# Kernel optimization log

Measured on AMD Instinct MI355X. Metric: run time of the kernel, lower is better.

The kernel has to match this reference:

```python
import jax, jax.numpy as jnp
import numpy as np

B, S, D = 8, 4096, 128


def setup_inputs() -> dict:
    key = jax.random.key(0)
    kx, kw = jax.random.split(key)
    x = jax.random.normal(kx, (B, S, D), dtype=jnp.float32)
    W = jax.random.normal(kw, (D, D), dtype=jnp.float32) * 0.05  # 'random_normal' init
    b = jnp.zeros((D,), dtype=jnp.float32)  # created in build() but unused in call()
    return {"x": x, "W": W, "b": b}


def reference(x, W, b):
    # q = a = x @ W  (both projections use the same weight in the source)
    q = jnp.einsum("bsd,de->bse", x, W)
    # scores = q @ a^T -> [B, S, S]; no 1/sqrt(d) scaling in the source
    scores = jnp.einsum("bsd,btd->bst", q, q)
    attn = jax.nn.softmax(scores, axis=-1)
    # output = attn @ inputs (values are the raw inputs, not a projection)
    out = jnp.einsum("bst,btd->bsd", attn, x)
    return out
```

## Files before the change

### kernel.cpp

```cpp
#include <hip/hip_runtime.h>

typedef unsigned short u16;
typedef unsigned int u32;
typedef short s16x8 __attribute__((ext_vector_type(8)));
typedef float f32x4 __attribute__((ext_vector_type(4)));
typedef float f32x16 __attribute__((ext_vector_type(16)));

#define B_  8
#define S_  4096
#define D_  128
#define SOFF 40.0f

#define VOFF  9216
#define BUFSZ 19456
#define SBUF  (2 * BUFSZ)
#define LDSZ  (4 * SBUF)

__device__ __forceinline__ u16 f2bf(float f) {
  union { float f; unsigned u; } v; v.f = f;
  unsigned r = v.u + 0x7fffu + ((v.u >> 16) & 1u);
  return (u16)(r >> 16);
}

__device__ __forceinline__ u32 pack_bf(float a, float b) {
  union { float f; u32 u; } ua, ub;
  ua.f = a; ub.f = b;
  return ((ua.u + 0x8000u) & 0xffff0000u) | ((ub.u + 0x8000u) >> 16);
}

__device__ __forceinline__ void async_cp16(const void* g, void* l) {
  __builtin_amdgcn_global_load_lds(
      (const __attribute__((address_space(1))) void*)g,
      (__attribute__((address_space(3))) void*)l, 16, 0, 0);
}

__global__ __launch_bounds__(256) void wprep_kernel(
    const float* __restrict__ W, u16* __restrict__ wtT)
{
  __shared__ u16 wb[128][136];
  int tid = threadIdx.x;
#pragma unroll
  for (int i = 0; i < 16; ++i) {
    int idx = i * 1024 + tid * 4;
    const float* p = W + idx;
    float a = p[0], b = p[1], c = p[2], d = p[3];
    int k = idx >> 7, n = idx & 127;
    *(u32*)(&wb[k][n])     = (u32)f2bf(a) | ((u32)f2bf(b) << 16);
    *(u32*)(&wb[k][n + 2]) = (u32)f2bf(c) | ((u32)f2bf(d) << 16);
  }
  __syncthreads();
#pragma unroll
  for (int i = 0; i < 32; ++i) {
    int oi = i * 256 + tid;
    int n = oi >> 6, kp = oi & 63;
    u32 v = (u32)wb[2 * kp][n] | ((u32)wb[2 * kp + 1][n] << 16);
    ((u32*)wtT)[n * 64 + kp] = v;
  }
}

__global__ __launch_bounds__(256) void prep_kernel(
    const float* __restrict__ x, const u16* __restrict__ wtT,
    u16* __restrict__ qb, u16* __restrict__ vT)
{
  __shared__ u16 xb[32][136];
  __shared__ u16 qs[32][136];
  const int tid  = threadIdx.x;
  const int b    = blockIdx.x & 7;
  const int m0   = (blockIdx.x >> 3) * 32;
  const int lane = tid & 63, wave = tid >> 6;
  const int l32  = lane & 31, hi = lane >> 5;

  const float* xg = x + ((size_t)b * S_ + m0) * D_;
#pragma unroll
  for (int i = 0; i < 4; ++i) {
    int idx = (i * 256 + tid) * 4;
    f32x4 v = *(const f32x4*)(xg + idx);
    int row = idx >> 7, col = idx & 127;
    *(u32*)(&xb[row][col])     = (u32)f2bf(v.x) | ((u32)f2bf(v.y) << 16);
    *(u32*)(&xb[row][col + 2]) = (u32)f2bf(v.z) | ((u32)f2bf(v.w) << 16);
  }
  __syncthreads();

  u16* vTb = vT + (size_t)b * D_ * S_;
#pragma unroll
  for (int i = 0; i < 8; ++i) {
    int oi = i * 256 + tid;
    int d = oi >> 4, jj = oi & 15, t = 2 * jj;
    u32 v = (u32)xb[t][d] | ((u32)xb[t + 1][d] << 16);
    int jjs = (jj & 9) | ((jj & 2) << 1) | ((jj & 4) >> 1);
    ((u32*)(vTb + (size_t)d * S_ + m0))[jjs] = v;
  }

  s16x8 a[8];
#pragma unroll
  for (int f = 0; f < 8; ++f)
    a[f] = *(const s16x8*)(&xb[l32][f * 16 + hi * 8]);
  f32x16 acc = (f32x16)(0.f);
#pragma unroll
  for (int f = 0; f < 8; ++f) {
    s16x8 bf = *(const s16x8*)(wtT + (size_t)(wave * 32 + l32) * 128 + f * 16 + hi * 8);
    acc = __builtin_amdgcn_mfma_f32_32x32x16_bf16(a[f], bf, acc, 0, 0, 0);
  }
#pragma unroll
  for (int r = 0; r < 16; ++r) {
    int row = (r & 3) + 8 * (r >> 2) + 4 * hi;
    qs[row][wave * 32 + l32] = f2bf(acc[r]);
  }
  __syncthreads();
  u16* qB = qb + ((size_t)b * S_ + m0) * D_;
#pragma unroll
  for (int i = 0; i < 8; ++i) {
    int oi = i * 256 + tid;
    int row = oi >> 6, jj = oi & 63;
    u32 v = (u32)qs[row][2 * jj] | ((u32)qs[row][2 * jj + 1] << 16);
    ((u32*)(qB + (size_t)row * D_))[jj] = v;
  }
}

__global__ __launch_bounds__(512, 2) void flash_kernel(
    const u16* __restrict__ qb, const u16* __restrict__ vT, float* __restrict__ out)
{
  __shared__ __align__(16) char smem[LDSZ];
  const int tid  = threadIdx.x;
  const int wave = tid >> 6, lane = tid & 63;
  const int w4   = wave & 3;
  const int half = wave >> 2;
  const int l32  = lane & 31, hi = lane >> 5;
  const int b    = blockIdx.x & 7;
  const int qt   = blockIdx.x >> 3;

  const u16* qbase = qb + (size_t)b * S_ * D_;
  const u16* vbase = vT + (size_t)b * D_ * S_;
  const u32 hbase = half ? (u32)(2 * SBUF) : 0u;
  const int koff  = half * 2048;

  const char* gp[5]; u32 lp[5]; u32 ksc[5];
#pragma unroll
  for (int sl = 0; sl < 5; ++sl) {
    int j = w4 + 4 * sl;
    if (j < 9) {
      u32 p = (u32)j * 64 + lane; if (p > 543u) p = 543u;
      u32 r = p / 17u; u32 cc = p - r * 17u; if (cc > 15u) cc = 15u;
      gp[sl]  = (const char*)qbase + (size_t)(koff + r) * 256 + cc * 16;
      ksc[sl] = 256; lp[sl] = hbase + (u32)j * 1024;
    } else if (j < 19) {
      u32 i = (u32)j - 9; u32 p = i * 64 + lane;
      u32 r = p / 5u; u32 cc = p - r * 5u; if (cc > 3u) cc = 3u;
      gp[sl]  = (const char*)vbase + (size_t)r * (S_ * 2) + (size_t)koff * 2 + cc * 16;
      ksc[sl] = 2; lp[sl] = hbase + VOFF + i * 1024;
    } else gp[sl] = nullptr;
  }

  s16x8 qf[8];
  {
    const u16* qr = qbase + (size_t)(qt * 128 + w4 * 32 + l32) * D_;
#pragma unroll
    for (int f = 0; f < 8; ++f)
      qf[f] = *(const s16x8*)(qr + f * 16 + hi * 8);
  }

  f32x16 o[4];
#pragma unroll
  for (int dt = 0; dt < 4; ++dt) o[dt] = (f32x16)(0.f);
  float l_i = 0.f;

#pragma unroll
  for (int sl = 0; sl < 5; ++sl)
    if (gp[sl]) async_cp16(gp[sl], smem + lp[sl]);
#pragma unroll
  for (int sl = 0; sl < 5; ++sl)
    if (gp[sl]) async_cp16(gp[sl] + (size_t)32 * ksc[sl], smem + lp[sl] + BUFSZ);
  __syncthreads();

  for (int t = 0; t < 32; ++t) {
    const int sb = t & 1;
    const char* baseA = smem + hbase + (sb ? SBUF : 0u);
    const char* baseB = baseA + BUFSZ;

    s16x8 kfA[8], kfB[8];
#pragma unroll
    for (int f = 0; f < 8; ++f) {
      kfA[f] = *(const s16x8*)(baseA + l32 * 272 + (f * 16 + hi * 8) * 2);
      kfB[f] = *(const s16x8*)(baseB + l32 * 272 + (f * 16 + hi * 8) * 2);
    }

    if (t < 31) {
      u32 k1 = (u32)(2 * t + 2) * 32;
      u32 dst = sb ? 0u : SBUF;
#pragma unroll
      for (int sl = 0; sl < 5; ++sl)
        if (gp[sl]) {
          async_cp16(gp[sl] + (size_t)k1 * ksc[sl], smem + lp[sl] + dst);
          async_cp16(gp[sl] + (size_t)(k1 + 32) * ksc[sl], smem + lp[sl] + dst + BUFSZ);
        }
    }

    f32x16 sA = (f32x16)(-SOFF), sB = (f32x16)(-SOFF);
    __builtin_amdgcn_s_setprio(1);
#pragma unroll
    for (int f = 0; f < 8; ++f) {
      sA = __builtin_amdgcn_mfma_f32_32x32x16_bf16(kfA[f], qf[f], sA, 0, 0, 0);
      sB = __builtin_amdgcn_mfma_f32_32x32x16_bf16(kfB[f], qf[f], sB, 0, 0, 0);
    }
    __builtin_amdgcn_s_setprio(0);

    const char* vbA = baseA + VOFF;
    const char* vbB = baseB + VOFF;
    s16x8 vfA[8], vfB[8];
#pragma unroll
    for (int dt = 0; dt < 4; ++dt)
#pragma unroll
      for (int kh = 0; kh < 2; ++kh) {
        vfA[dt * 2 + kh] = *(const s16x8*)(vbA + (dt * 32 + l32) * 80 + kh * 32 + hi * 16);
        vfB[dt * 2 + kh] = *(const s16x8*)(vbB + (dt * 32 + l32) * 80 + kh * 32 + hi * 16);
      }

    float eA[16], eB[16];
#pragma unroll
    for (int r = 0; r < 16; ++r) { eA[r] = __expf(sA[r]); eB[r] = __expf(sB[r]); }

    float psA = (((eA[0]+eA[1])+(eA[2]+eA[3]))+((eA[4]+eA[5])+(eA[6]+eA[7])))
              + (((eA[8]+eA[9])+(eA[10]+eA[11]))+((eA[12]+eA[13])+(eA[14]+eA[15])));
    float psB = (((eB[0]+eB[1])+(eB[2]+eB[3]))+((eB[4]+eB[5])+(eB[6]+eB[7])))
              + (((eB[8]+eB[9])+(eB[10]+eB[11]))+((eB[12]+eB[13])+(eB[14]+eB[15])));
    float ps = psA + psB;
    ps += __shfl_xor(ps, 32, 64);
    l_i += ps;

    union { u32 u[4]; s16x8 v; } pf0A, pf1A, pf0B, pf1B;
    pf0A.u[0] = pack_bf(eA[1],  eA[0]);
    pf0A.u[1] = pack_bf(eA[3],  eA[2]);
    pf0A.u[2] = pack_bf(eA[5],  eA[4]);
    pf0A.u[3] = pack_bf(eA[7],  eA[6]);
    pf1A.u[0] = pack_bf(eA[9],  eA[8]);
    pf1A.u[1] = pack_bf(eA[11], eA[10]);
    pf1A.u[2] = pack_bf(eA[13], eA[12]);
    pf1A.u[3] = pack_bf(eA[15], eA[14]);
    pf0B.u[0] = pack_bf(eB[1],  eB[0]);
    pf0B.u[1] = pack_bf(eB[3],  eB[2]);
    pf0B.u[2] = pack_bf(eB[5],  eB[4]);
    pf0B.u[3] = pack_bf(eB[7],  eB[6]);
    pf1B.u[0] = pack_bf(eB[9],  eB[8]);
    pf1B.u[1] = pack_bf(eB[11], eB[10]);
    pf1B.u[2] = pack_bf(eB[13], eB[12]);
    pf1B.u[3] = pack_bf(eB[15], eB[14]);

    __builtin_amdgcn_s_setprio(1);
#pragma unroll
    for (int dt = 0; dt < 4; ++dt) {
      o[dt] = __builtin_amdgcn_mfma_f32_32x32x16_bf16(vfA[dt * 2 + 0], pf0A.v, o[dt], 0, 0, 0);
      o[dt] = __builtin_amdgcn_mfma_f32_32x32x16_bf16(vfA[dt * 2 + 1], pf1A.v, o[dt], 0, 0, 0);
      o[dt] = __builtin_amdgcn_mfma_f32_32x32x16_bf16(vfB[dt * 2 + 0], pf0B.v, o[dt], 0, 0, 0);
      o[dt] = __builtin_amdgcn_mfma_f32_32x32x16_bf16(vfB[dt * 2 + 1], pf1B.v, o[dt], 0, 0, 0);
    }
    __builtin_amdgcn_s_setprio(0);

    __syncthreads();
  }

  float (*lo)[132] = (float (*)[132])smem;
  float* ll = (float*)(smem + 128 * 132 * 4);

  if (half == 1) {
#pragma unroll
    for (int dt = 0; dt < 4; ++dt)
#pragma unroll
      for (int r = 0; r < 16; ++r) {
        int d = dt * 32 + (r & 3) + 8 * (r >> 2) + 4 * hi;
        lo[w4 * 32 + l32][d] = o[dt][r];
      }
    if (hi == 0) ll[w4 * 32 + l32] = l_i;
  }
  __syncthreads();
  if (half == 0) {
    float lt  = l_i + ll[w4 * 32 + l32];
    float inv = 1.0f / lt;
#pragma unroll
    for (int dt = 0; dt < 4; ++dt)
#pragma unroll
      for (int r = 0; r < 16; ++r) {
        int d = dt * 32 + (r & 3) + 8 * (r >> 2) + 4 * hi;
        float* p = &lo[w4 * 32 + l32][d];
        *p = (o[dt][r] + *p) * inv;
      }
  }
  __syncthreads();
  {
    float* ob = out + ((size_t)b * S_ + qt * 128) * D_;
#pragma unroll
    for (int i = 0; i < 8; ++i) {
      int flat = (i * 512 + tid) * 4;
      int row = flat >> 7, d = flat & 127;
      *(f32x4*)(ob + flat) = *(const f32x4*)(&lo[row][d]);
    }
  }
}

extern "C" void kernel_launch(void* const* d_in, const int* in_sizes, int n_in,
                              void* d_out, int out_size, void* d_ws, size_t ws_size,
                              hipStream_t stream) {
  const float* x = (const float*)d_in[0];
  const float* W = (const float*)d_in[1];
  float* out = (float*)d_out;

  u16* qb  = (u16*)d_ws;
  u16* vT  = qb + (size_t)B_ * S_ * D_;
  u16* wtT = vT + (size_t)B_ * D_ * S_;

  wprep_kernel<<<1, 256, 0, stream>>>(W, wtT);
  prep_kernel<<<8 * (S_ / 32), 256, 0, stream>>>(x, wtT, qb, vT);
  flash_kernel<<<8 * (S_ / 128), 512, 0, stream>>>(qb, vT, out);
}
```

Baseline: 164.4 us.

## Fuse weight prep, projection and flash attention into one cooperative kernel

Merges the three launches (weight bf16 transpose, Q projection/V transpose, flash attention) into a single cooperative kernel with a grid-wide sync between the prep phase and the attention phase. Each block rebuilds the transposed bf16 weight in LDS itself and projects its own 128 rows before syncing. This removes two kernel launches and their gaps, at the cost of redundant per-block weight conversion and a grid barrier that requires all 256 blocks to be co-resident, with the old three-kernel path kept as a fallback if the cooperative launch fails.

```diff
diff --git a/kernel.cpp b/kernel.cpp
--- a/kernel.cpp
+++ b/kernel.cpp
@@ -1,4 +1,5 @@
 #include <hip/hip_runtime.h>
+#include <hip/hip_cooperative_groups.h>
 
 typedef unsigned short u16;
 typedef unsigned int u32;
@@ -34,93 +35,10 @@
       (__attribute__((address_space(3))) void*)l, 16, 0, 0);
 }
 
-__global__ __launch_bounds__(256) void wprep_kernel(
-    const float* __restrict__ W, u16* __restrict__ wtT)
+__device__ __forceinline__ void flash_body(
+    const u16* __restrict__ qb, const u16* __restrict__ vT,
+    float* __restrict__ out, char* smem)
 {
-  __shared__ u16 wb[128][136];
-  int tid = threadIdx.x;
-#pragma unroll
-  for (int i = 0; i < 16; ++i) {
-    int idx = i * 1024 + tid * 4;
-    const float* p = W + idx;
-    float a = p[0], b = p[1], c = p[2], d = p[3];
-    int k = idx >> 7, n = idx & 127;
-    *(u32*)(&wb[k][n])     = (u32)f2bf(a) | ((u32)f2bf(b) << 16);
-    *(u32*)(&wb[k][n + 2]) = (u32)f2bf(c) | ((u32)f2bf(d) << 16);
-  }
-  __syncthreads();
-#pragma unroll
-  for (int i = 0; i < 32; ++i) {
-    int oi = i * 256 + tid;
-    int n = oi >> 6, kp = oi & 63;
-    u32 v = (u32)wb[2 * kp][n] | ((u32)wb[2 * kp + 1][n] << 16);
-    ((u32*)wtT)[n * 64 + kp] = v;
-  }
-}
-
-__global__ __launch_bounds__(256) void prep_kernel(
-    const float* __restrict__ x, const u16* __restrict__ wtT,
-    u16* __restrict__ qb, u16* __restrict__ vT)
-{
-  __shared__ u16 xb[32][136];
-  __shared__ u16 qs[32][136];
-  const int tid  = threadIdx.x;
-  const int b    = blockIdx.x & 7;
-  const int m0   = (blockIdx.x >> 3) * 32;
-  const int lane = tid & 63, wave = tid >> 6;
-  const int l32  = lane & 31, hi = lane >> 5;
-
-  const float* xg = x + ((size_t)b * S_ + m0) * D_;
-#pragma unroll
-  for (int i = 0; i < 4; ++i) {
-    int idx = (i * 256 + tid) * 4;
-    f32x4 v = *(const f32x4*)(xg + idx);
-    int row = idx >> 7, col = idx & 127;
-    *(u32*)(&xb[row][col])     = (u32)f2bf(v.x) | ((u32)f2bf(v.y) << 16);
-    *(u32*)(&xb[row][col + 2]) = (u32)f2bf(v.z) | ((u32)f2bf(v.w) << 16);
-  }
-  __syncthreads();
-
-  u16* vTb = vT + (size_t)b * D_ * S_;
-#pragma unroll
-  for (int i = 0; i < 8; ++i) {
-    int oi = i * 256 + tid;
-    int d = oi >> 4, jj = oi & 15, t = 2 * jj;
-    u32 v = (u32)xb[t][d] | ((u32)xb[t + 1][d] << 16);
-    int jjs = (jj & 9) | ((jj & 2) << 1) | ((jj & 4) >> 1);
-    ((u32*)(vTb + (size_t)d * S_ + m0))[jjs] = v;
-  }
-
-  s16x8 a[8];
-#pragma unroll
-  for (int f = 0; f < 8; ++f)
-    a[f] = *(const s16x8*)(&xb[l32][f * 16 + hi * 8]);
-  f32x16 acc = (f32x16)(0.f);
-#pragma unroll
-  for (int f = 0; f < 8; ++f) {
-    s16x8 bf = *(const s16x8*)(wtT + (size_t)(wave * 32 + l32) * 128 + f * 16 + hi * 8);
-    acc = __builtin_amdgcn_mfma_f32_32x32x16_bf16(a[f], bf, acc, 0, 0, 0);
-  }
-#pragma unroll
-  for (int r = 0; r < 16; ++r) {
-    int row = (r & 3) + 8 * (r >> 2) + 4 * hi;
-    qs[row][wave * 32 + l32] = f2bf(acc[r]);
-  }
-  __syncthreads();
-  u16* qB = qb + ((size_t)b * S_ + m0) * D_;
-#pragma unroll
-  for (int i = 0; i < 8; ++i) {
-    int oi = i * 256 + tid;
-    int row = oi >> 6, jj = oi & 63;
-    u32 v = (u32)qs[row][2 * jj] | ((u32)qs[row][2 * jj + 1] << 16);
-    ((u32*)(qB + (size_t)row * D_))[jj] = v;
-  }
-}
-
-__global__ __launch_bounds__(512, 2) void flash_kernel(
-    const u16* __restrict__ qb, const u16* __restrict__ vT, float* __restrict__ out)
-{
-  __shared__ __align__(16) char smem[LDSZ];
   const int tid  = threadIdx.x;
   const int wave = tid >> 6, lane = tid & 63;
   const int w4   = wave & 3;
@@ -296,6 +214,191 @@
   }
 }
 
+__global__ __launch_bounds__(512, 2) void fused_kernel(
+    const float* __restrict__ x, const float* __restrict__ W,
+    u16* __restrict__ qb, u16* __restrict__ vT, float* __restrict__ out)
+{
+  __shared__ __align__(16) char smem[LDSZ];
+  const int tid  = threadIdx.x;
+  const int b    = blockIdx.x & 7;
+  const int qt   = blockIdx.x >> 3;
+  const int wave = tid >> 6, lane = tid & 63;
+  const int l32  = lane & 31, hi = lane >> 5;
+
+  u16 (*wtL)[136] = (u16 (*)[136])smem;
+  u16 (*wb)[136]  = (u16 (*)[136])(smem + 69632);
+#pragma unroll
+  for (int i = 0; i < 8; ++i) {
+    int idx = i * 2048 + tid * 4;
+    const float* p = W + idx;
+    float a = p[0], b2 = p[1], c = p[2], d = p[3];
+    int k = idx >> 7, n = idx & 127;
+    *(u32*)(&wb[k][n])     = (u32)f2bf(a) | ((u32)f2bf(b2) << 16);
+    *(u32*)(&wb[k][n + 2]) = (u32)f2bf(c) | ((u32)f2bf(d) << 16);
+  }
+  __syncthreads();
+#pragma unroll
+  for (int i = 0; i < 16; ++i) {
+    int oi = i * 512 + tid;
+    int n = oi >> 6, kp = oi & 63;
+    u32 v = (u32)wb[2 * kp][n] | ((u32)wb[2 * kp + 1][n] << 16);
+    *(u32*)(&wtL[n][2 * kp]) = v;
+  }
+
+  u16 (*xb)[136] = (u16 (*)[136])(smem + 34816);
+  u16 (*qs)[136] = (u16 (*)[136])(smem + 52224);
+  const int tw = wave >> 2;
+  const int nt = wave & 3;
+  u16* vTb = vT + (size_t)b * D_ * S_;
+
+#pragma unroll
+  for (int p2 = 0; p2 < 2; ++p2) {
+    const int rowb = qt * 128 + p2 * 64;
+    const float* xg = x + ((size_t)b * S_ + rowb) * D_;
+#pragma unroll
+    for (int i = 0; i < 4; ++i) {
+      int idx = (i * 512 + tid) * 4;
+      f32x4 v = *(const f32x4*)(xg + idx);
+      int row = idx >> 7, col = idx & 127;
+      *(u32*)(&xb[row][col])     = (u32)f2bf(v.x) | ((u32)f2bf(v.y) << 16);
+      *(u32*)(&xb[row][col + 2]) = (u32)f2bf(v.z) | ((u32)f2bf(v.w) << 16);
+    }
+    __syncthreads();
+
+#pragma unroll
+    for (int i = 0; i < 8; ++i) {
+      int oi = i * 512 + tid;
+      int d = oi >> 5, r5 = oi & 31;
+      int tt = r5 >> 4, jj = r5 & 15;
+      u32 v = (u32)xb[tt * 32 + 2 * jj][d] | ((u32)xb[tt * 32 + 2 * jj + 1][d] << 16);
+      int jjs = (jj & 9) | ((jj & 2) << 1) | ((jj & 4) >> 1);
+      ((u32*)(vTb + (size_t)d * S_ + rowb + tt * 32))[jjs] = v;
+    }
+
+    s16x8 a[8];
+#pragma unroll
+    for (int f = 0; f < 8; ++f)
+      a[f] = *(const s16x8*)(&xb[tw * 32 + l32][f * 16 + hi * 8]);
+    f32x16 acc = (f32x16)(0.f);
+#pragma unroll
+    for (int f = 0; f < 8; ++f) {
+      s16x8 bf = *(const s16x8*)(&wtL[nt * 32 + l32][f * 16 + hi * 8]);
+      acc = __builtin_amdgcn_mfma_f32_32x32x16_bf16(a[f], bf, acc, 0, 0, 0);
+    }
+#pragma unroll
+    for (int r = 0; r < 16; ++r) {
+      int row = (r & 3) + 8 * (r >> 2) + 4 * hi;
+      qs[tw * 32 + row][nt * 32 + l32] = f2bf(acc[r]);
+    }
+    __syncthreads();
+
+    u16* qB = qb + ((size_t)b * S_ + rowb) * D_;
+#pragma unroll
+    for (int i = 0; i < 8; ++i) {
+      int oi = i * 512 + tid;
+      int row = oi >> 6, jj = oi & 63;
+      u32 v = (u32)qs[row][2 * jj] | ((u32)qs[row][2 * jj + 1] << 16);
+      ((u32*)(qB + (size_t)row * D_))[jj] = v;
+    }
+    __syncthreads();
+  }
+
+  __threadfence();
+  cooperative_groups::this_grid().sync();
+
+  flash_body(qb, vT, out, smem);
+}
+
+__global__ __launch_bounds__(256) void wprep_kernel(
+    const float* __restrict__ W, u16* __restrict__ wtT)
+{
+  __shared__ u16 wb[128][136];
+  int tid = threadIdx.x;
+#pragma unroll
+  for (int i = 0; i < 16; ++i) {
+    int idx = i * 1024 + tid * 4;
+    const float* p = W + idx;
+    float a = p[0], b = p[1], c = p[2], d = p[3];
+    int k = idx >> 7, n = idx & 127;
+    *(u32*)(&wb[k][n])     = (u32)f2bf(a) | ((u32)f2bf(b) << 16);
+    *(u32*)(&wb[k][n + 2]) = (u32)f2bf(c) | ((u32)f2bf(d) << 16);
+  }
+  __syncthreads();
+#pragma unroll
+  for (int i = 0; i < 32; ++i) {
+    int oi = i * 256 + tid;
+    int n = oi >> 6, kp = oi & 63;
+    u32 v = (u32)wb[2 * kp][n] | ((u32)wb[2 * kp + 1][n] << 16);
+    ((u32*)wtT)[n * 64 + kp] = v;
+  }
+}
+
+__global__ __launch_bounds__(256) void prep_kernel(
+    const float* __restrict__ x, const u16* __restrict__ wtT,
+    u16* __restrict__ qb, u16* __restrict__ vT)
+{
+  __shared__ u16 xb[32][136];
+  __shared__ u16 qs[32][136];
+  const int tid  = threadIdx.x;
+  const int b    = blockIdx.x & 7;
+  const int m0   = (blockIdx.x >> 3) * 32;
+  const int lane = tid & 63, wave = tid >> 6;
+  const int l32  = lane & 31, hi = lane >> 5;
+
+  const float* xg = x + ((size_t)b * S_ + m0) * D_;
+#pragma unroll
+  for (int i = 0; i < 4; ++i) {
+    int idx = (i * 256 + tid) * 4;
+    f32x4 v = *(const f32x4*)(xg + idx);
+    int row = idx >> 7, col = idx & 127;
+    *(u32*)(&xb[row][col])     = (u32)f2bf(v.x) | ((u32)f2bf(v.y) << 16);
+    *(u32*)(&xb[row][col + 2]) = (u32)f2bf(v.z) | ((u32)f2bf(v.w) << 16);
+  }
+  __syncthreads();
+
+  u16* vTb = vT + (size_t)b * D_ * S_;
+#pragma unroll
+  for (int i = 0; i < 8; ++i) {
+    int oi = i * 256 + tid;
+    int d = oi >> 4, jj = oi & 15, t = 2 * jj;
+    u32 v = (u32)xb[t][d] | ((u32)xb[t + 1][d] << 16);
+    int jjs = (jj & 9) | ((jj & 2) << 1) | ((jj & 4) >> 1);
+    ((u32*)(vTb + (size_t)d * S_ + m0))[jjs] = v;
+  }
+
+  s16x8 a[8];
+#pragma unroll
+  for (int f = 0; f < 8; ++f)
+    a[f] = *(const s16x8*)(&xb[l32][f * 16 + hi * 8]);
+  f32x16 acc = (f32x16)(0.f);
+#pragma unroll
+  for (int f = 0; f < 8; ++f) {
+    s16x8 bf = *(const s16x8*)(wtT + (size_t)(wave * 32 + l32) * 128 + f * 16 + hi * 8);
+    acc = __builtin_amdgcn_mfma_f32_32x32x16_bf16(a[f], bf, acc, 0, 0, 0);
+  }
+#pragma unroll
+  for (int r = 0; r < 16; ++r) {
+    int row = (r & 3) + 8 * (r >> 2) + 4 * hi;
+    qs[row][wave * 32 + l32] = f2bf(acc[r]);
+  }
+  __syncthreads();
+  u16* qB = qb + ((size_t)b * S_ + m0) * D_;
+#pragma unroll
+  for (int i = 0; i < 8; ++i) {
+    int oi = i * 256 + tid;
+    int row = oi >> 6, jj = oi & 63;
+    u32 v = (u32)qs[row][2 * jj] | ((u32)qs[row][2 * jj + 1] << 16);
+    ((u32*)(qB + (size_t)row * D_))[jj] = v;
+  }
+}
+
+__global__ __launch_bounds__(512, 2) void flash_kernel(
+    const u16* __restrict__ qb, const u16* __restrict__ vT, float* __restrict__ out)
+{
+  __shared__ __align__(16) char smem[LDSZ];
+  flash_body(qb, vT, out, smem);
+}
+
 extern "C" void kernel_launch(void* const* d_in, const int* in_sizes, int n_in,
                               void* d_out, int out_size, void* d_ws, size_t ws_size,
                               hipStream_t stream) {
@@ -307,7 +410,12 @@
   u16* vT  = qb + (size_t)B_ * S_ * D_;
   u16* wtT = vT + (size_t)B_ * D_ * S_;
 
-  wprep_kernel<<<1, 256, 0, stream>>>(W, wtT);
-  prep_kernel<<<8 * (S_ / 32), 256, 0, stream>>>(x, wtT, qb, vT);
-  flash_kernel<<<8 * (S_ / 128), 512, 0, stream>>>(qb, vT, out);
-}
+  void* params[] = { (void*)&x, (void*)&W, (void*)&qb, (void*)&vT, (void*)&out };
+  hipError_t err = hipLaunchCooperativeKernel(
+      (const void*)fused_kernel, dim3(8 * (S_ / 128)), dim3(512), params, 0, stream);
+  if (err != hipSuccess) {
+    wprep_kernel<<<1, 256, 0, stream>>>(W, wtT);
+    prep_kernel<<<8 * (S_ / 32), 256, 0, stream>>>(x, wtT, qb, vT);
+    flash_kernel<<<8 * (S_ / 128), 512, 0, stream>>>(qb, vT, out);
+  }
+}
```

After: 228.7 us. 1.39x slower.
